# Kernel optimization log

Hardware: AMD Instinct MI355X
Metric: run time of the kernel (lower is better)

## Reference

```python
import jax, jax.numpy as jnp
import numpy as np

N = 50000          # num_nodes
E = 1600000        # num directed edges
IN_C = 128         # in_channels
OUT_C = 128        # out_channels
HEADS = 8
HFD = OUT_C // HEADS  # head_feat_dim = 16
NEG_SLOPE = 0.2


def setup_inputs() -> dict:
    key = jax.random.key(0)
    k1, k2, k3, k4, k5 = jax.random.split(key, 5)
    node_feats = jax.random.normal(k1, (N, IN_C), dtype=jnp.float32)
    edge_index = jax.random.randint(k2, (2, E), 0, N, dtype=jnp.int64)
    # parameters (xavier-ish scale, kept small so exp() stays in range)
    W = jax.random.normal(k3, (OUT_C, IN_C), dtype=jnp.float32) * (1.0 / np.sqrt(IN_C))
    a_left = jax.random.normal(k4, (HFD, HEADS), dtype=jnp.float32) * 0.1
    a_right = jax.random.normal(k5, (HFD, HEADS), dtype=jnp.float32) * 0.1
    bias = jnp.zeros((OUT_C,), dtype=jnp.float32)
    return {"node_feats": node_feats, "edge_index": edge_index,
            "W": W, "a_left": a_left, "a_right": a_right, "bias": bias}


def reference(node_feats, edge_index, W, a_left, a_right, bias):
    n = node_feats.shape[0]
    # embedding: Linear without bias, then split into heads -> [n, h, c]
    emb = (node_feats @ W.T).reshape(n, HEADS, HFD)
    # per-node attention logit halves: sum_c emb[n,h,c] * a[c,h] -> [n, h]
    left = jnp.einsum('nhc,ch->nh', emb, a_left)
    right = jnp.einsum('nhc,ch->nh', emb, a_right)
    src = edge_index[0]
    dst = edge_index[1]
    # edge logit: score(src, dst) uses a_left on src, a_right on dst
    e = left[src] + right[dst]                       # [E, h]
    e = jnp.where(e >= 0, e, NEG_SLOPE * e)          # leaky relu(0.2)
    w = jnp.exp(e)                                   # [E, h] (module uses raw exp)
    denom = jax.ops.segment_sum(w, dst, num_segments=n)  # [n, h]
    attn = w / denom[dst]                            # [E, h]
    msg = emb[src] * attn[:, :, None]                # [E, h, c]
    out = jax.ops.segment_sum(msg, dst, num_segments=n)  # [n, h, c]
    # concat heads + bias
    out = out.reshape(n, HEADS * HFD) + bias
    return out
```

## Files before the change

kernel.cpp:

```cpp
#include <hip/hip_runtime.h>
#include <hip/hip_bf16.h>

#define N_NODES 50000
#define N_EDGES 1600000
#define HEADS 8
#define HFD 16
#define CH 128

#define PART 128
#define NB 391
#define BCAP 5120
#define PA_T 512
#define PA_CHUNK 3200
#define PA_PER 7
#define PA_BLOCKS 500

typedef __bf16 bf16x8 __attribute__((ext_vector_type(8)));
typedef __bf16 bf16x4 __attribute__((ext_vector_type(4)));
typedef float f32x4 __attribute__((ext_vector_type(4)));

__device__ __forceinline__ float bf_lo(unsigned u) { return __uint_as_float(u << 16); }
__device__ __forceinline__ float bf_hi(unsigned u) { return __uint_as_float(u & 0xffff0000u); }

__global__ __launch_bounds__(256) void k_splitw(const float* __restrict__ W,
                                                const float* __restrict__ aL,
                                                const float* __restrict__ aR,
                                                __bf16* __restrict__ Whi,
                                                __bf16* __restrict__ Wlo,
                                                __bf16* __restrict__ Vhi,
                                                __bf16* __restrict__ Vlo,
                                                int* __restrict__ bucket_cnt) {
  int t = blockIdx.x * 256 + threadIdx.x;
  if (t < NB) bucket_cnt[t] = 0;
  if (t < CH * CH / 4) {
    f32x4 v = ((const f32x4*)W)[t];
    bf16x4 h, l;
#pragma unroll
    for (int i = 0; i < 4; ++i) {
      __bf16 hb = (__bf16)v[i];
      h[i] = hb;
      l[i] = (__bf16)(v[i] - (float)hb);
    }
    ((bf16x4*)Whi)[t] = h;
    ((bf16x4*)Wlo)[t] = l;
  }
  if (t < 16 * CH) {
    int j = t >> 7;
    int k = t & 127;
    int h = j & 7;
    const float* a = (j < 8) ? aL : aR;
    float v = 0.f;
#pragma unroll
    for (int c = 0; c < HFD; ++c) v += W[(h * HFD + c) * CH + k] * a[c * HEADS + h];
    __bf16 hb = (__bf16)v;
    Vhi[t] = hb;
    Vlo[t] = (__bf16)(v - (float)hb);
  }
}

__global__ __launch_bounds__(64) void k_emb(const float* __restrict__ X,
                                            const __bf16* __restrict__ Whi,
                                            const __bf16* __restrict__ Wlo,
                                            const __bf16* __restrict__ Vhi,
                                            const __bf16* __restrict__ Vlo,
                                            __bf16* __restrict__ embb,
                                            float* __restrict__ leftp,
                                            float* __restrict__ rightp) {
  int ntile = blockIdx.x;
  int lane = threadIdx.x;
  int c = lane & 15, quad = lane >> 4;
  const float* xp = X + (size_t)(ntile * 16 + c) * CH + quad * 8;
  bf16x8 xh[4], xl[4];
#pragma unroll
  for (int ks = 0; ks < 4; ++ks) {
    float4 x0 = *(const float4*)(xp + ks * 32);
    float4 x1 = *(const float4*)(xp + ks * 32 + 4);
    float xv[8] = {x0.x, x0.y, x0.z, x0.w, x1.x, x1.y, x1.z, x1.w};
#pragma unroll
    for (int j = 0; j < 8; ++j) {
      __bf16 hb = (__bf16)xv[j];
      xh[ks][j] = hb;
      xl[ks][j] = (__bf16)(xv[j] - (float)hb);
    }
  }
#pragma unroll
  for (int h = 0; h < HEADS; ++h) {
    const __bf16* wp = Whi + (size_t)(h * 16 + c) * CH + quad * 8;
    const __bf16* wlp = Wlo + (size_t)(h * 16 + c) * CH + quad * 8;
    f32x4 acc = {0.f, 0.f, 0.f, 0.f};
#pragma unroll
    for (int ks = 0; ks < 4; ++ks) {
      bf16x8 wh = *(const bf16x8*)(wp + ks * 32);
      bf16x8 wl = *(const bf16x8*)(wlp + ks * 32);
      acc = __builtin_amdgcn_mfma_f32_16x16x32_bf16(xl[ks], wh, acc, 0, 0, 0);
      acc = __builtin_amdgcn_mfma_f32_16x16x32_bf16(xh[ks], wl, acc, 0, 0, 0);
      acc = __builtin_amdgcn_mfma_f32_16x16x32_bf16(xh[ks], wh, acc, 0, 0, 0);
    }
#pragma unroll
    for (int r = 0; r < 4; ++r) {
      int node = ntile * 16 + quad * 4 + r;
      embb[(size_t)node * CH + h * HFD + c] = (__bf16)acc[r];
    }
  }
  {
    const __bf16* vp = Vhi + (size_t)c * CH + quad * 8;
    const __bf16* vlp = Vlo + (size_t)c * CH + quad * 8;
    f32x4 acc = {0.f, 0.f, 0.f, 0.f};
#pragma unroll
    for (int ks = 0; ks < 4; ++ks) {
      bf16x8 vh = *(const bf16x8*)(vp + ks * 32);
      bf16x8 vl = *(const bf16x8*)(vlp + ks * 32);
      acc = __builtin_amdgcn_mfma_f32_16x16x32_bf16(xl[ks], vh, acc, 0, 0, 0);
      acc = __builtin_amdgcn_mfma_f32_16x16x32_bf16(xh[ks], vl, acc, 0, 0, 0);
      acc = __builtin_amdgcn_mfma_f32_16x16x32_bf16(xh[ks], vh, acc, 0, 0, 0);
    }
#pragma unroll
    for (int r = 0; r < 4; ++r) {
      int node = ntile * 16 + quad * 4 + r;
      if (c < 8) leftp[node * HEADS + c] = acc[r];
      else rightp[node * HEADS + (c - 8)] = acc[r];
    }
  }
}

__global__ __launch_bounds__(PA_T) void k_bucket(const int* __restrict__ ei,
                                                 int* __restrict__ bucket_cnt,
                                                 unsigned* __restrict__ ebuf) {
  __shared__ unsigned sp[PA_CHUNK];
  __shared__ int hist[NB];
  __shared__ int lcur[NB];
  __shared__ int wbase[NB];
  __shared__ int scn[PA_T];
  int t = threadIdx.x;
  int base = blockIdx.x * PA_CHUNK;
  for (int i = t; i < NB; i += PA_T) hist[i] = 0;
  __syncthreads();
  unsigned pk[PA_PER];
#pragma unroll
  for (int i = 0; i < PA_PER; ++i) {
    int e = t + i * PA_T;
    pk[i] = 0xffffffffu;
    if (e < PA_CHUNK) {
      int src = ei[base + e];
      int dst = ei[N_EDGES + base + e];
      pk[i] = ((unsigned)(dst >> 7) << 23) | ((unsigned)(dst & 127) << 16) |
              (unsigned)src;
      atomicAdd(&hist[dst >> 7], 1);
    }
  }
  __syncthreads();
  scn[t] = (t < NB) ? hist[t] : 0;
  __syncthreads();
  int val = scn[t];
  for (int d = 1; d < PA_T; d <<= 1) {
    int o = (t >= d) ? scn[t - d] : 0;
    __syncthreads();
    val += o;
    scn[t] = val;
    __syncthreads();
  }
  if (t < NB) {
    int hv = hist[t];
    int lstart = val - hv;
    lcur[t] = lstart;
    int prior = hv ? atomicAdd(&bucket_cnt[t], hv) : 0;
    wbase[t] = t * BCAP + prior - lstart;
  }
  __syncthreads();
#pragma unroll
  for (int i = 0; i < PA_PER; ++i) {
    if (pk[i] != 0xffffffffu) {
      int b = pk[i] >> 23;
      int pos = atomicAdd(&lcur[b], 1);
      sp[pos] = pk[i];
    }
  }
  __syncthreads();
  for (int i = t; i < PA_CHUNK; i += PA_T) {
    unsigned p = sp[i];
    int b = p >> 23;
    int slot = wbase[b] + i;
    if (slot < (b + 1) * BCAP) ebuf[slot] = p;
  }
}

__global__ __launch_bounds__(512) void k_aggr(const int* __restrict__ bucket_cnt,
                                              const unsigned* __restrict__ ebuf,
                                              const __bf16* __restrict__ embb,
                                              const float* __restrict__ leftp,
                                              const float* __restrict__ rightp,
                                              const float* __restrict__ bias,
                                              float* __restrict__ out) {
  __shared__ unsigned short su[BCAP];
  __shared__ int hist[PART];
  __shared__ int pfx[PART];
  __shared__ int cur[PART];
  int b = blockIdx.x >> 1;
  int half = blockIdx.x & 1;
  int t = threadIdx.x;
  int cnt = bucket_cnt[b];
  if (cnt > BCAP) cnt = BCAP;
  int ebase = b * BCAP;
  if (t < PART) hist[t] = 0;
  __syncthreads();
  for (int e = t; e < cnt; e += 512)
    atomicAdd(&hist[(ebuf[ebase + e] >> 16) & 127], 1);
  __syncthreads();
  if (t < PART) pfx[t] = hist[t];
  __syncthreads();
  for (int d = 1; d < PART; d <<= 1) {
    int v = 0;
    if (t < PART) { v = pfx[t]; if (t >= d) v += pfx[t - d]; }
    __syncthreads();
    if (t < PART) pfx[t] = v;
    __syncthreads();
  }
  if (t < PART) {
    int excl = pfx[t] - hist[t];
    pfx[t] = excl;
    cur[t] = excl;
  }
  __syncthreads();
  for (int e = t; e < cnt; e += 512) {
    unsigned p = ebuf[ebase + e];
    int pos = atomicAdd(&cur[(p >> 16) & 127], 1);
    su[pos] = (unsigned short)(p & 0xffffu);
  }
  __syncthreads();

  int wv = t >> 6;
  int lane = t & 63;
  int g = lane >> 4;
  int m = lane & 15;
  int h = m >> 1;
#pragma unroll
  for (int k = 0; k < 8; ++k) {
    int dl = half * 64 + wv * 8 + k;
    int dst = b * PART + dl;
    bool valid = dst < N_NODES;
    int beg = pfx[dl];
    int cd = hist[dl];
    float r = valid ? rightp[dst * HEADS + h] : 0.f;
    float acc[8] = {0.f, 0.f, 0.f, 0.f, 0.f, 0.f, 0.f, 0.f};
    float dsum = 0.f;
    for (int e0 = 0; e0 < cd; e0 += 8) {
      int i0 = e0 + g, i1 = e0 + 4 + g;
      bool a0 = i0 < cd, a1 = i1 < cd;
      int s0 = su[beg + (a0 ? i0 : 0)];
      int s1 = su[beg + (a1 ? i1 : 0)];
      uint4 u0 = ((const uint4*)(embb + (size_t)s0 * CH))[m];
      uint4 u1 = ((const uint4*)(embb + (size_t)s1 * CH))[m];
      float l0 = leftp[s0 * HEADS + h];
      float l1 = leftp[s1 * HEADS + h];
      float x0 = l0 + r;
      x0 = (x0 >= 0.f) ? x0 : 0.2f * x0;
      float w0 = a0 ? __expf(x0) : 0.f;
      float x1 = l1 + r;
      x1 = (x1 >= 0.f) ? x1 : 0.2f * x1;
      float w1 = a1 ? __expf(x1) : 0.f;
      dsum += w0 + w1;
      acc[0] += w0 * bf_lo(u0.x) + w1 * bf_lo(u1.x);
      acc[1] += w0 * bf_hi(u0.x) + w1 * bf_hi(u1.x);
      acc[2] += w0 * bf_lo(u0.y) + w1 * bf_lo(u1.y);
      acc[3] += w0 * bf_hi(u0.y) + w1 * bf_hi(u1.y);
      acc[4] += w0 * bf_lo(u0.z) + w1 * bf_lo(u1.z);
      acc[5] += w0 * bf_hi(u0.z) + w1 * bf_hi(u1.z);
      acc[6] += w0 * bf_lo(u0.w) + w1 * bf_lo(u1.w);
      acc[7] += w0 * bf_hi(u0.w) + w1 * bf_hi(u1.w);
    }
#pragma unroll
    for (int mask = 16; mask <= 32; mask <<= 1) {
      dsum += __shfl_xor(dsum, mask);
#pragma unroll
      for (int j = 0; j < 8; ++j) acc[j] += __shfl_xor(acc[j], mask);
    }
    if (g == 0 && valid) {
      float inv = (dsum > 0.f) ? 1.0f / dsum : 0.f;
      float4 b0 = ((const float4*)bias)[2 * m];
      float4 b1 = ((const float4*)bias)[2 * m + 1];
      float4 o0 = {acc[0] * inv + b0.x, acc[1] * inv + b0.y,
                   acc[2] * inv + b0.z, acc[3] * inv + b0.w};
      float4 o1 = {acc[4] * inv + b1.x, acc[5] * inv + b1.y,
                   acc[6] * inv + b1.z, acc[7] * inv + b1.w};
      ((float4*)(out + (size_t)dst * CH))[2 * m] = o0;
      ((float4*)(out + (size_t)dst * CH))[2 * m + 1] = o1;
    }
  }
}

extern "C" void kernel_launch(void* const* d_in, const int* in_sizes, int n_in,
                              void* d_out, int out_size, void* d_ws, size_t ws_size,
                              hipStream_t stream) {
  const float* X = (const float*)d_in[0];
  const int* ei = (const int*)d_in[1];
  const float* W = (const float*)d_in[2];
  const float* al = (const float*)d_in[3];
  const float* ar = (const float*)d_in[4];
  const float* bias = (const float*)d_in[5];
  float* out = (float*)d_out;

  unsigned* ebuf = (unsigned*)d_ws;
  __bf16* embb = (__bf16*)(ebuf + (size_t)NB * BCAP);
  __bf16* Whi = embb + (size_t)N_NODES * CH;
  __bf16* Wlo = Whi + CH * CH;
  __bf16* Vhi = Wlo + CH * CH;
  __bf16* Vlo = Vhi + 16 * CH;
  float* leftp = (float*)(Vlo + 16 * CH);
  float* rightp = leftp + (size_t)N_NODES * HEADS;
  int* bucket_cnt = (int*)(rightp + (size_t)N_NODES * HEADS);

  k_splitw<<<16, 256, 0, stream>>>(W, al, ar, Whi, Wlo, Vhi, Vlo, bucket_cnt);
  k_bucket<<<PA_BLOCKS, PA_T, 0, stream>>>(ei, bucket_cnt, ebuf);
  k_emb<<<N_NODES / 16, 64, 0, stream>>>(X, Whi, Wlo, Vhi, Vlo, embb, leftp, rightp);
  k_aggr<<<NB * 2, 512, 0, stream>>>(bucket_cnt, ebuf, embb, leftp, rightp, bias, out);
}
```

Before: 213.8 us.

## Split aggregation into quarter-bucket tasks with XCD-aware mapping and software pipelining

The aggregation kernel now runs each 128-destination bucket as four 32-destination tasks on 256-thread blocks. Each block filters the bucket's edges down to its quarter, using vectorized uint4 reads of the edge buffer and a wave-shuffle scan in place of the shared-memory scan. Block indices are remapped round-robin across groups of 8, and the per-destination edge loop is double-buffered so gathers for the next 8 edges are issued before the current ones are consumed. The aim is more, smaller blocks for better occupancy and latency hiding. The cost is that every block rereads the whole bucket's edge list, and a new QCAP clamp could drop edges if a quarter receives more than 1536 edges.

```diff
diff --git a/kernel.cpp b/kernel.cpp
--- a/kernel.cpp
+++ b/kernel.cpp
@@ -14,6 +14,11 @@
 #define PA_CHUNK 3200
 #define PA_PER 7
 #define PA_BLOCKS 500
+
+#define QPART 32
+#define QCAP 1536
+#define AG_TASKS (NB * 4)
+#define AG_BLOCKS 1568
 
 typedef __bf16 bf16x8 __attribute__((ext_vector_type(8)));
 typedef __bf16 bf16x4 __attribute__((ext_vector_type(4)));
@@ -184,47 +189,67 @@
   }
 }
 
-__global__ __launch_bounds__(512) void k_aggr(const int* __restrict__ bucket_cnt,
+__global__ __launch_bounds__(256) void k_aggr(const int* __restrict__ bucket_cnt,
                                               const unsigned* __restrict__ ebuf,
                                               const __bf16* __restrict__ embb,
                                               const float* __restrict__ leftp,
                                               const float* __restrict__ rightp,
                                               const float* __restrict__ bias,
                                               float* __restrict__ out) {
-  __shared__ unsigned short su[BCAP];
-  __shared__ int hist[PART];
-  __shared__ int pfx[PART];
-  __shared__ int cur[PART];
-  int b = blockIdx.x >> 1;
-  int half = blockIdx.x & 1;
+  __shared__ unsigned short su[QCAP];
+  __shared__ int hist[QPART];
+  __shared__ int pfx[QPART];
+  __shared__ int cur[QPART];
+  int T = (blockIdx.x & 7) * (AG_BLOCKS / 8) + (blockIdx.x >> 3);
+  if (T >= AG_TASKS) return;
+  int b = T >> 2;
+  int q = T & 3;
   int t = threadIdx.x;
   int cnt = bucket_cnt[b];
   if (cnt > BCAP) cnt = BCAP;
   int ebase = b * BCAP;
-  if (t < PART) hist[t] = 0;
-  __syncthreads();
-  for (int e = t; e < cnt; e += 512)
-    atomicAdd(&hist[(ebuf[ebase + e] >> 16) & 127], 1);
-  __syncthreads();
-  if (t < PART) pfx[t] = hist[t];
-  __syncthreads();
-  for (int d = 1; d < PART; d <<= 1) {
-    int v = 0;
-    if (t < PART) { v = pfx[t]; if (t >= d) v += pfx[t - d]; }
-    __syncthreads();
-    if (t < PART) pfx[t] = v;
-    __syncthreads();
-  }
-  if (t < PART) {
-    int excl = pfx[t] - hist[t];
-    pfx[t] = excl;
-    cur[t] = excl;
-  }
-  __syncthreads();
-  for (int e = t; e < cnt; e += 512) {
-    unsigned p = ebuf[ebase + e];
-    int pos = atomicAdd(&cur[(p >> 16) & 127], 1);
-    su[pos] = (unsigned short)(p & 0xffffu);
+  if (t < QPART) hist[t] = 0;
+  __syncthreads();
+  for (int e4 = t * 4; e4 < cnt; e4 += 1024) {
+    uint4 pp = *(const uint4*)(ebuf + ebase + e4);
+    unsigned pj[4] = {pp.x, pp.y, pp.z, pp.w};
+#pragma unroll
+    for (int j = 0; j < 4; ++j) {
+      if (e4 + j < cnt) {
+        int dl = (pj[j] >> 16) & 127;
+        if ((dl >> 5) == q) atomicAdd(&hist[dl & 31], 1);
+      }
+    }
+  }
+  __syncthreads();
+  if (t < 64) {
+    int v = (t < QPART) ? hist[t] : 0;
+#pragma unroll
+    for (int d = 1; d < QPART; d <<= 1) {
+      int o = __shfl_up(v, d);
+      if (t >= d) v += o;
+    }
+    if (t < QPART) {
+      int ex = v - hist[t];
+      pfx[t] = ex;
+      cur[t] = ex;
+    }
+  }
+  __syncthreads();
+  for (int e4 = t * 4; e4 < cnt; e4 += 1024) {
+    uint4 pp = *(const uint4*)(ebuf + ebase + e4);
+    unsigned pj[4] = {pp.x, pp.y, pp.z, pp.w};
+#pragma unroll
+    for (int j = 0; j < 4; ++j) {
+      if (e4 + j < cnt) {
+        unsigned p = pj[j];
+        int dl = (p >> 16) & 127;
+        if ((dl >> 5) == q) {
+          int pos = atomicAdd(&cur[dl & 31], 1);
+          if (pos < QCAP) su[pos] = (unsigned short)(p & 0xffffu);
+        }
+      }
+    }
   }
   __syncthreads();
 
@@ -233,40 +258,64 @@
   int g = lane >> 4;
   int m = lane & 15;
   int h = m >> 1;
-#pragma unroll
+#pragma unroll 1
   for (int k = 0; k < 8; ++k) {
-    int dl = half * 64 + wv * 8 + k;
-    int dst = b * PART + dl;
+    int dl = wv * 8 + k;
+    int dst = b * PART + q * QPART + dl;
     bool valid = dst < N_NODES;
     int beg = pfx[dl];
     int cd = hist[dl];
+    if (beg + cd > QCAP) cd = QCAP - beg;
     float r = valid ? rightp[dst * HEADS + h] : 0.f;
     float acc[8] = {0.f, 0.f, 0.f, 0.f, 0.f, 0.f, 0.f, 0.f};
     float dsum = 0.f;
-    for (int e0 = 0; e0 < cd; e0 += 8) {
-      int i0 = e0 + g, i1 = e0 + 4 + g;
-      bool a0 = i0 < cd, a1 = i1 < cd;
-      int s0 = su[beg + (a0 ? i0 : 0)];
-      int s1 = su[beg + (a1 ? i1 : 0)];
-      uint4 u0 = ((const uint4*)(embb + (size_t)s0 * CH))[m];
-      uint4 u1 = ((const uint4*)(embb + (size_t)s1 * CH))[m];
-      float l0 = leftp[s0 * HEADS + h];
-      float l1 = leftp[s1 * HEADS + h];
-      float x0 = l0 + r;
-      x0 = (x0 >= 0.f) ? x0 : 0.2f * x0;
-      float w0 = a0 ? __expf(x0) : 0.f;
-      float x1 = l1 + r;
-      x1 = (x1 >= 0.f) ? x1 : 0.2f * x1;
-      float w1 = a1 ? __expf(x1) : 0.f;
-      dsum += w0 + w1;
-      acc[0] += w0 * bf_lo(u0.x) + w1 * bf_lo(u1.x);
-      acc[1] += w0 * bf_hi(u0.x) + w1 * bf_hi(u1.x);
-      acc[2] += w0 * bf_lo(u0.y) + w1 * bf_lo(u1.y);
-      acc[3] += w0 * bf_hi(u0.y) + w1 * bf_hi(u1.y);
-      acc[4] += w0 * bf_lo(u0.z) + w1 * bf_lo(u1.z);
-      acc[5] += w0 * bf_hi(u0.z) + w1 * bf_hi(u1.z);
-      acc[6] += w0 * bf_lo(u0.w) + w1 * bf_lo(u1.w);
-      acc[7] += w0 * bf_hi(u0.w) + w1 * bf_hi(u1.w);
+    if (cd > 0) {
+      int sA0, sA1, sB0, sB1;
+      uint4 uA0, uA1, uB0, uB1;
+      float lA0, lA1, lB0, lB1;
+#define STAGE(E0, s0, s1, u0, u1, l0, l1)                          \
+      {                                                            \
+        int i0 = (E0) + g, i1 = (E0) + 4 + g;                      \
+        s0 = su[beg + ((i0 < cd) ? i0 : 0)];                       \
+        s1 = su[beg + ((i1 < cd) ? i1 : 0)];                       \
+        u0 = ((const uint4*)(embb + (size_t)s0 * CH))[m];          \
+        u1 = ((const uint4*)(embb + (size_t)s1 * CH))[m];          \
+        l0 = leftp[s0 * HEADS + h];                                \
+        l1 = leftp[s1 * HEADS + h];                                \
+      }
+#define CONSUME(E0, u0, u1, l0, l1)                                \
+      {                                                            \
+        bool a0 = (E0) + g < cd, a1 = (E0) + 4 + g < cd;           \
+        float x0 = l0 + r;                                         \
+        x0 = (x0 >= 0.f) ? x0 : 0.2f * x0;                         \
+        float w0 = a0 ? __expf(x0) : 0.f;                          \
+        float x1 = l1 + r;                                         \
+        x1 = (x1 >= 0.f) ? x1 : 0.2f * x1;                         \
+        float w1 = a1 ? __expf(x1) : 0.f;                          \
+        dsum += w0 + w1;                                           \
+        acc[0] += w0 * bf_lo(u0.x) + w1 * bf_lo(u1.x);             \
+        acc[1] += w0 * bf_hi(u0.x) + w1 * bf_hi(u1.x);             \
+        acc[2] += w0 * bf_lo(u0.y) + w1 * bf_lo(u1.y);             \
+        acc[3] += w0 * bf_hi(u0.y) + w1 * bf_hi(u1.y);             \
+        acc[4] += w0 * bf_lo(u0.z) + w1 * bf_lo(u1.z);             \
+        acc[5] += w0 * bf_hi(u0.z) + w1 * bf_hi(u1.z);             \
+        acc[6] += w0 * bf_lo(u0.w) + w1 * bf_lo(u1.w);             \
+        acc[7] += w0 * bf_hi(u0.w) + w1 * bf_hi(u1.w);             \
+      }
+      STAGE(0, sA0, sA1, uA0, uA1, lA0, lA1);
+      int e0 = 0;
+      while (true) {
+        if (e0 + 8 < cd) STAGE(e0 + 8, sB0, sB1, uB0, uB1, lB0, lB1);
+        CONSUME(e0, uA0, uA1, lA0, lA1);
+        e0 += 8;
+        if (e0 >= cd) break;
+        if (e0 + 8 < cd) STAGE(e0 + 8, sA0, sA1, uA0, uA1, lA0, lA1);
+        CONSUME(e0, uB0, uB1, lB0, lB1);
+        e0 += 8;
+        if (e0 >= cd) break;
+      }
+#undef STAGE
+#undef CONSUME
     }
 #pragma unroll
     for (int mask = 16; mask <= 32; mask <<= 1) {
@@ -312,5 +361,5 @@
   k_splitw<<<16, 256, 0, stream>>>(W, al, ar, Whi, Wlo, Vhi, Vlo, bucket_cnt);
   k_bucket<<<PA_BLOCKS, PA_T, 0, stream>>>(ei, bucket_cnt, ebuf);
   k_emb<<<N_NODES / 16, 64, 0, stream>>>(X, Whi, Wlo, Vhi, Vlo, embb, leftp, rightp);
-  k_aggr<<<NB * 2, 512, 0, stream>>>(bucket_cnt, ebuf, embb, leftp, rightp, bias, out);
-}
+  k_aggr<<<AG_BLOCKS, 256, 0, stream>>>(bucket_cnt, ebuf, embb, leftp, rightp, bias, out);
+}
```

Result: faster. 204.1 us (-4.5%).

## Use 32-node buckets with balanced edge-pair scheduling and software-pipelined aggregation

Applied to the files above, without the earlier changes.

Buckets shrink from 128 to 32 destination nodes, so there are more, smaller aggregation blocks, each with 256 threads. Each block builds a schedule of edge pairs and splits it evenly across 16 quarter-wave teams, so high-degree nodes no longer stall a wave. The gather loop double-buffers the embedding and left-logit loads to hide memory latency. The bucket kernel's scan handles 1563 bins by giving each thread four of them. Risks include more global atomics on bucket counters, edges silently dropped when a bucket exceeds its capacity of 1280, and the extra cost of building the schedule.

```diff
diff --git a/kernel.cpp b/kernel.cpp
--- a/kernel.cpp
+++ b/kernel.cpp
@@ -7,13 +7,15 @@
 #define HFD 16
 #define CH 128
 
-#define PART 128
-#define NB 391
-#define BCAP 5120
+#define NB2 1563
+#define ECAP2 1280
 #define PA_T 512
 #define PA_CHUNK 3200
 #define PA_PER 7
 #define PA_BLOCKS 500
+
+#define AG_BLOCKS 1568
+#define SCHED_CAP 672
 
 typedef __bf16 bf16x8 __attribute__((ext_vector_type(8)));
 typedef __bf16 bf16x4 __attribute__((ext_vector_type(4)));
@@ -31,7 +33,7 @@
                                                 __bf16* __restrict__ Vlo,
                                                 int* __restrict__ bucket_cnt) {
   int t = blockIdx.x * 256 + threadIdx.x;
-  if (t < NB) bucket_cnt[t] = 0;
+  if (t < NB2) bucket_cnt[t] = 0;
   if (t < CH * CH / 4) {
     f32x4 v = ((const f32x4*)W)[t];
     bf16x4 h, l;
@@ -127,13 +129,13 @@
                                                  int* __restrict__ bucket_cnt,
                                                  unsigned* __restrict__ ebuf) {
   __shared__ unsigned sp[PA_CHUNK];
-  __shared__ int hist[NB];
-  __shared__ int lcur[NB];
-  __shared__ int wbase[NB];
+  __shared__ int hist[NB2 + 1];
+  __shared__ int lcur[NB2];
+  __shared__ int wbase[NB2];
   __shared__ int scn[PA_T];
   int t = threadIdx.x;
   int base = blockIdx.x * PA_CHUNK;
-  for (int i = t; i < NB; i += PA_T) hist[i] = 0;
+  for (int i = t; i < NB2; i += PA_T) hist[i] = 0;
   __syncthreads();
   unsigned pk[PA_PER];
 #pragma unroll
@@ -143,13 +145,18 @@
     if (e < PA_CHUNK) {
       int src = ei[base + e];
       int dst = ei[N_EDGES + base + e];
-      pk[i] = ((unsigned)(dst >> 7) << 23) | ((unsigned)(dst & 127) << 16) |
-              (unsigned)src;
-      atomicAdd(&hist[dst >> 7], 1);
-    }
-  }
-  __syncthreads();
-  scn[t] = (t < NB) ? hist[t] : 0;
+      pk[i] = ((unsigned)dst << 16) | (unsigned)src;
+      atomicAdd(&hist[dst >> 5], 1);
+    }
+  }
+  __syncthreads();
+  int b4 = t * 4;
+  int h0 = (b4 < NB2) ? hist[b4] : 0;
+  int h1 = (b4 + 1 < NB2) ? hist[b4 + 1] : 0;
+  int h2 = (b4 + 2 < NB2) ? hist[b4 + 2] : 0;
+  int h3 = (b4 + 3 < NB2) ? hist[b4 + 3] : 0;
+  int s4 = h0 + h1 + h2 + h3;
+  scn[t] = s4;
   __syncthreads();
   int val = scn[t];
   for (int d = 1; d < PA_T; d <<= 1) {
@@ -159,18 +166,25 @@
     scn[t] = val;
     __syncthreads();
   }
-  if (t < NB) {
-    int hv = hist[t];
-    int lstart = val - hv;
-    lcur[t] = lstart;
-    int prior = hv ? atomicAdd(&bucket_cnt[t], hv) : 0;
-    wbase[t] = t * BCAP + prior - lstart;
+  {
+    int lst = val - s4;
+    int run[4] = {h0, h1, h2, h3};
+#pragma unroll
+    for (int j = 0; j < 4; ++j) {
+      int b = b4 + j;
+      if (b < NB2) {
+        lcur[b] = lst;
+        int prior = run[j] ? atomicAdd(&bucket_cnt[b], run[j]) : 0;
+        wbase[b] = b * ECAP2 + prior - lst;
+        lst += run[j];
+      }
+    }
   }
   __syncthreads();
 #pragma unroll
   for (int i = 0; i < PA_PER; ++i) {
     if (pk[i] != 0xffffffffu) {
-      int b = pk[i] >> 23;
+      int b = pk[i] >> 21;
       int pos = atomicAdd(&lcur[b], 1);
       sp[pos] = pk[i];
     }
@@ -178,112 +192,191 @@
   __syncthreads();
   for (int i = t; i < PA_CHUNK; i += PA_T) {
     unsigned p = sp[i];
-    int b = p >> 23;
+    int b = p >> 21;
     int slot = wbase[b] + i;
-    if (slot < (b + 1) * BCAP) ebuf[slot] = p;
+    if (slot < (b + 1) * ECAP2) ebuf[slot] = p;
   }
 }
 
-__global__ __launch_bounds__(512) void k_aggr(const int* __restrict__ bucket_cnt,
+__global__ __launch_bounds__(256) void k_aggr(const int* __restrict__ bucket_cnt,
                                               const unsigned* __restrict__ ebuf,
                                               const __bf16* __restrict__ embb,
                                               const float* __restrict__ leftp,
                                               const float* __restrict__ rightp,
                                               const float* __restrict__ bias,
                                               float* __restrict__ out) {
-  __shared__ unsigned short su[BCAP];
-  __shared__ int hist[PART];
-  __shared__ int pfx[PART];
-  __shared__ int cur[PART];
-  int b = blockIdx.x >> 1;
-  int half = blockIdx.x & 1;
+  __shared__ unsigned short su[ECAP2];
+  __shared__ int hist[32];
+  __shared__ int pfx[32];
+  __shared__ int cur[32];
+  __shared__ int poff[32];
+  __shared__ int tb[17];
+  __shared__ float r_lds[256];
+  __shared__ unsigned sched[SCHED_CAP];
+  __shared__ int Ptot;
+
+  int T = (blockIdx.x & 7) * 196 + (blockIdx.x >> 3);
+  if (T >= NB2) return;
   int t = threadIdx.x;
-  int cnt = bucket_cnt[b];
-  if (cnt > BCAP) cnt = BCAP;
-  int ebase = b * BCAP;
-  if (t < PART) hist[t] = 0;
-  __syncthreads();
-  for (int e = t; e < cnt; e += 512)
-    atomicAdd(&hist[(ebuf[ebase + e] >> 16) & 127], 1);
-  __syncthreads();
-  if (t < PART) pfx[t] = hist[t];
-  __syncthreads();
-  for (int d = 1; d < PART; d <<= 1) {
-    int v = 0;
-    if (t < PART) { v = pfx[t]; if (t >= d) v += pfx[t - d]; }
-    __syncthreads();
-    if (t < PART) pfx[t] = v;
-    __syncthreads();
-  }
-  if (t < PART) {
-    int excl = pfx[t] - hist[t];
-    pfx[t] = excl;
-    cur[t] = excl;
-  }
-  __syncthreads();
-  for (int e = t; e < cnt; e += 512) {
-    unsigned p = ebuf[ebase + e];
-    int pos = atomicAdd(&cur[(p >> 16) & 127], 1);
-    su[pos] = (unsigned short)(p & 0xffffu);
-  }
-  __syncthreads();
-
-  int wv = t >> 6;
+  int dstbase = T * 32;
+  int cnt = bucket_cnt[T];
+  if (cnt > ECAP2) cnt = ECAP2;
+  const unsigned* wnd = ebuf + (size_t)T * ECAP2;
+
+  if (t < 32) hist[t] = 0;
+  {
+    int dst = dstbase + (t >> 3);
+    r_lds[t] = (dst < N_NODES) ? rightp[dst * HEADS + (t & 7)] : 0.f;
+  }
+  __syncthreads();
+  for (int e = t; e < cnt; e += 256) atomicAdd(&hist[(wnd[e] >> 16) & 31], 1);
+  __syncthreads();
+  if (t < 64) {
+    int hv = (t < 32) ? hist[t] : 0;
+    int v = hv;
+#pragma unroll
+    for (int d = 1; d < 32; d <<= 1) {
+      int o = __shfl_up(v, d);
+      if ((t & 63) >= d) v += o;
+    }
+    if (t < 32) { pfx[t] = v - hv; cur[t] = v - hv; }
+    int np = (t < 32) ? (hv + 1) >> 1 : 0;
+    int pv = np;
+#pragma unroll
+    for (int d = 1; d < 32; d <<= 1) {
+      int o = __shfl_up(pv, d);
+      if ((t & 63) >= d) pv += o;
+    }
+    if (t < 32) poff[t] = pv - np;
+    if (t == 31) Ptot = pv;
+  }
+  __syncthreads();
+  int P = Ptot;
+  if (t == 0) {
+    tb[0] = 0;
+    int curw = 0;
+    if (P > 0) {
+      for (int dl = 0; dl < 32; ++dl) {
+        int w = (int)((16LL * poff[dl]) / P);
+        if (w > 15) w = 15;
+        while (curw < w) tb[++curw] = poff[dl];
+      }
+    }
+    while (curw < 16) tb[++curw] = P;
+  }
+  if (t < 32) {
+    int cd = hist[t], basee = pfx[t], po = poff[t];
+    int e = 0;
+    for (int e2 = 0; e2 < cd; e2 += 2, ++e) {
+      unsigned nv2 = (cd - e2 > 1) ? 1u : 0u;
+      sched[po + e] = (unsigned)(basee + e2) | ((unsigned)t << 11) |
+                      ((e == 0) ? (1u << 16) : 0u) | (nv2 << 17);
+    }
+  }
+  __syncthreads();
+  for (int e = t; e < cnt; e += 256) {
+    unsigned p = wnd[e];
+    int dl = (p >> 16) & 31;
+    int pos = atomicAdd(&cur[dl], 1);
+    if (pos < ECAP2) su[pos] = (unsigned short)(p & 0xffffu);
+  }
+  __syncthreads();
+
   int lane = t & 63;
-  int g = lane >> 4;
+  int tm = (t >> 6) * 4 + (lane >> 4);
   int m = lane & 15;
   int h = m >> 1;
-#pragma unroll
-  for (int k = 0; k < 8; ++k) {
-    int dl = half * 64 + wv * 8 + k;
-    int dst = b * PART + dl;
-    bool valid = dst < N_NODES;
-    int beg = pfx[dl];
-    int cd = hist[dl];
-    float r = valid ? rightp[dst * HEADS + h] : 0.f;
-    float acc[8] = {0.f, 0.f, 0.f, 0.f, 0.f, 0.f, 0.f, 0.f};
-    float dsum = 0.f;
-    for (int e0 = 0; e0 < cd; e0 += 8) {
-      int i0 = e0 + g, i1 = e0 + 4 + g;
-      bool a0 = i0 < cd, a1 = i1 < cd;
-      int s0 = su[beg + (a0 ? i0 : 0)];
-      int s1 = su[beg + (a1 ? i1 : 0)];
-      uint4 u0 = ((const uint4*)(embb + (size_t)s0 * CH))[m];
-      uint4 u1 = ((const uint4*)(embb + (size_t)s1 * CH))[m];
-      float l0 = leftp[s0 * HEADS + h];
-      float l1 = leftp[s1 * HEADS + h];
-      float x0 = l0 + r;
-      x0 = (x0 >= 0.f) ? x0 : 0.2f * x0;
-      float w0 = a0 ? __expf(x0) : 0.f;
-      float x1 = l1 + r;
-      x1 = (x1 >= 0.f) ? x1 : 0.2f * x1;
-      float w1 = a1 ? __expf(x1) : 0.f;
-      dsum += w0 + w1;
-      acc[0] += w0 * bf_lo(u0.x) + w1 * bf_lo(u1.x);
-      acc[1] += w0 * bf_hi(u0.x) + w1 * bf_hi(u1.x);
-      acc[2] += w0 * bf_lo(u0.y) + w1 * bf_lo(u1.y);
-      acc[3] += w0 * bf_hi(u0.y) + w1 * bf_hi(u1.y);
-      acc[4] += w0 * bf_lo(u0.z) + w1 * bf_lo(u1.z);
-      acc[5] += w0 * bf_hi(u0.z) + w1 * bf_hi(u1.z);
-      acc[6] += w0 * bf_lo(u0.w) + w1 * bf_lo(u1.w);
-      acc[7] += w0 * bf_hi(u0.w) + w1 * bf_hi(u1.w);
-    }
-#pragma unroll
-    for (int mask = 16; mask <= 32; mask <<= 1) {
-      dsum += __shfl_xor(dsum, mask);
-#pragma unroll
-      for (int j = 0; j < 8; ++j) acc[j] += __shfl_xor(acc[j], mask);
-    }
-    if (g == 0 && valid) {
-      float inv = (dsum > 0.f) ? 1.0f / dsum : 0.f;
-      float4 b0 = ((const float4*)bias)[2 * m];
-      float4 b1 = ((const float4*)bias)[2 * m + 1];
-      float4 o0 = {acc[0] * inv + b0.x, acc[1] * inv + b0.y,
-                   acc[2] * inv + b0.z, acc[3] * inv + b0.w};
-      float4 o1 = {acc[4] * inv + b1.x, acc[5] * inv + b1.y,
-                   acc[6] * inv + b1.z, acc[7] * inv + b1.w};
-      ((float4*)(out + (size_t)dst * CH))[2 * m] = o0;
-      ((float4*)(out + (size_t)dst * CH))[2 * m + 1] = o1;
+  float4 bb0 = ((const float4*)bias)[2 * m];
+  float4 bb1 = ((const float4*)bias)[2 * m + 1];
+
+  int pi = tb[tm], pe = tb[tm + 1];
+  float acc0 = 0.f, acc1 = 0.f, acc2 = 0.f, acc3 = 0.f;
+  float acc4 = 0.f, acc5 = 0.f, acc6 = 0.f, acc7 = 0.f;
+  float dsum = 0.f, r = 0.f;
+  int prev = -1;
+
+  unsigned eA = 0, eB = 0;
+  uint4 uA0, uA1, uB0, uB1;
+  float lA0 = 0.f, lA1 = 0.f, lB0 = 0.f, lB1 = 0.f;
+
+#define STAGE(E, U0, U1, L0, L1)                                     \
+  {                                                                  \
+    E = sched[pi];                                                   \
+    int ba = E & 0x7ff;                                              \
+    int s0 = su[ba];                                                 \
+    int s1 = su[ba + ((E >> 17) & 1)];                               \
+    U0 = ((const uint4*)(embb + (size_t)s0 * CH))[m];                \
+    U1 = ((const uint4*)(embb + (size_t)s1 * CH))[m];                \
+    L0 = leftp[s0 * HEADS + h];                                      \
+    L1 = leftp[s1 * HEADS + h];                                      \
+  }
+
+#define COMMIT()                                                     \
+  {                                                                  \
+    float inv = (dsum > 0.f) ? 1.0f / dsum : 0.f;                    \
+    float* op = out + (size_t)(dstbase + prev) * CH;                 \
+    float4 o0 = {acc0 * inv + bb0.x, acc1 * inv + bb0.y,             \
+                 acc2 * inv + bb0.z, acc3 * inv + bb0.w};            \
+    float4 o1 = {acc4 * inv + bb1.x, acc5 * inv + bb1.y,             \
+                 acc6 * inv + bb1.z, acc7 * inv + bb1.w};            \
+    ((float4*)op)[2 * m] = o0;                                       \
+    ((float4*)op)[2 * m + 1] = o1;                                   \
+  }
+
+#define CONSUME(E, U0, U1, L0, L1)                                   \
+  {                                                                  \
+    if (E & (1u << 16)) {                                            \
+      if (prev >= 0) COMMIT();                                       \
+      prev = (E >> 11) & 31;                                         \
+      r = r_lds[prev * 8 + h];                                       \
+      acc0 = acc1 = acc2 = acc3 = acc4 = acc5 = acc6 = acc7 = 0.f;   \
+      dsum = 0.f;                                                    \
+    }                                                                \
+    float x0 = L0 + r;                                               \
+    x0 = (x0 >= 0.f) ? x0 : 0.2f * x0;                               \
+    float w0 = __expf(x0);                                           \
+    float x1 = L1 + r;                                               \
+    x1 = (x1 >= 0.f) ? x1 : 0.2f * x1;                               \
+    float w1 = ((E >> 17) & 1) ? __expf(x1) : 0.f;                   \
+    dsum += w0 + w1;                                                 \
+    acc0 += w0 * bf_lo(U0.x) + w1 * bf_lo(U1.x);                     \
+    acc1 += w0 * bf_hi(U0.x) + w1 * bf_hi(U1.x);                     \
+    acc2 += w0 * bf_lo(U0.y) + w1 * bf_lo(U1.y);                     \
+    acc3 += w0 * bf_hi(U0.y) + w1 * bf_hi(U1.y);                     \
+    acc4 += w0 * bf_lo(U0.z) + w1 * bf_lo(U1.z);                     \
+    acc5 += w0 * bf_hi(U0.z) + w1 * bf_hi(U1.z);                     \
+    acc6 += w0 * bf_lo(U0.w) + w1 * bf_lo(U1.w);                     \
+    acc7 += w0 * bf_hi(U0.w) + w1 * bf_hi(U1.w);                     \
+  }
+
+  bool vA = pi < pe;
+  if (vA) STAGE(eA, uA0, uA1, lA0, lA1);
+  pi++;
+  bool vB = pi < pe;
+  if (vB) STAGE(eB, uB0, uB1, lB0, lB1);
+  pi++;
+  while (__any(vA)) {
+    if (vA) CONSUME(eA, uA0, uA1, lA0, lA1);
+    vA = pi < pe;
+    if (vA) STAGE(eA, uA0, uA1, lA0, lA1);
+    pi++;
+    if (!__any(vB)) break;
+    if (vB) CONSUME(eB, uB0, uB1, lB0, lB1);
+    vB = pi < pe;
+    if (vB) STAGE(eB, uB0, uB1, lB0, lB1);
+    pi++;
+  }
+  if (prev >= 0) COMMIT();
+#undef STAGE
+#undef COMMIT
+#undef CONSUME
+
+  for (int z = t; z < 32 * 32; z += 256) {
+    int dl = z >> 5, c4 = z & 31;
+    if (hist[dl] == 0) {
+      int dst = dstbase + dl;
+      if (dst < N_NODES)
+        ((float4*)(out + (size_t)dst * CH))[c4] = ((const float4*)bias)[c4];
     }
   }
 }
@@ -300,7 +393,7 @@
   float* out = (float*)d_out;
 
   unsigned* ebuf = (unsigned*)d_ws;
-  __bf16* embb = (__bf16*)(ebuf + (size_t)NB * BCAP);
+  __bf16* embb = (__bf16*)(ebuf + (size_t)NB2 * ECAP2);
   __bf16* Whi = embb + (size_t)N_NODES * CH;
   __bf16* Wlo = Whi + CH * CH;
   __bf16* Vhi = Wlo + CH * CH;
@@ -312,5 +405,5 @@
   k_splitw<<<16, 256, 0, stream>>>(W, al, ar, Whi, Wlo, Vhi, Vlo, bucket_cnt);
   k_bucket<<<PA_BLOCKS, PA_T, 0, stream>>>(ei, bucket_cnt, ebuf);
   k_emb<<<N_NODES / 16, 64, 0, stream>>>(X, Whi, Wlo, Vhi, Vlo, embb, leftp, rightp);
-  k_aggr<<<NB * 2, 512, 0, stream>>>(bucket_cnt, ebuf, embb, leftp, rightp, bias, out);
+  k_aggr<<<AG_BLOCKS, 256, 0, stream>>>(bucket_cnt, ebuf, embb, leftp, rightp, bias, out);
 }
```

New measurement: 245.7 us. +14.9%, slower.
